# Kernel tuning notes

Measured on AMD Instinct MI355X. Metric: run time of the kernel, lower is better.

Reference implementation:

```python
import jax, jax.numpy as jnp
import numpy as np

D_MODEL = 1024
N_HEADS = 16
D_FF = 4096
EPS = 1e-5


def _linear_init(key, fan_in, fan_out):
    # torch nn.Linear default: U(-1/sqrt(fan_in), 1/sqrt(fan_in))
    k1, k2 = jax.random.split(key)
    bound = 1.0 / np.sqrt(fan_in)
    W = jax.random.uniform(k1, (fan_in, fan_out), minval=-bound, maxval=bound, dtype=jnp.float32)
    b = jax.random.uniform(k2, (fan_out,), minval=-bound, maxval=bound, dtype=jnp.float32)
    return W, b


def setup_inputs() -> dict:
    key = jax.random.key(0)
    ks = jax.random.split(key, 8)
    x = jax.random.normal(ks[0], (4, 2048, D_MODEL), dtype=jnp.float32)
    Wq, bq = _linear_init(ks[1], D_MODEL, D_MODEL)
    Wk, bk = _linear_init(ks[2], D_MODEL, D_MODEL)
    Wv, bv = _linear_init(ks[3], D_MODEL, D_MODEL)
    Wo, bo = _linear_init(ks[4], D_MODEL, D_MODEL)
    W1, b1 = _linear_init(ks[5], D_MODEL, D_FF)
    W2, b2 = _linear_init(ks[6], D_FF, D_MODEL)
    g1 = jnp.ones((D_MODEL,), jnp.float32); be1 = jnp.zeros((D_MODEL,), jnp.float32)
    g2 = jnp.ones((D_MODEL,), jnp.float32); be2 = jnp.zeros((D_MODEL,), jnp.float32)
    return {"x": x, "Wq": Wq, "bq": bq, "Wk": Wk, "bk": bk, "Wv": Wv, "bv": bv,
            "Wo": Wo, "bo": bo, "g1": g1, "be1": be1, "W1": W1, "b1": b1,
            "W2": W2, "b2": b2, "g2": g2, "be2": be2}


def _layernorm(x, g, b):
    mu = jnp.mean(x, axis=-1, keepdims=True)
    var = jnp.mean(jnp.square(x - mu), axis=-1, keepdims=True)
    return (x - mu) * jax.lax.rsqrt(var + EPS) * g + b


def reference(x, Wq, bq, Wk, bk, Wv, bv, Wo, bo, g1, be1, W1, b1, W2, b2, g2, be2):
    B, T, D = x.shape
    H, dk = N_HEADS, D // N_HEADS
    # projections -> [B, H, T, dk]
    def split_heads(y):
        return y.reshape(B, T, H, dk).transpose(0, 2, 1, 3)
    Q = split_heads(x @ Wq + bq)
    K = split_heads(x @ Wk + bk)
    V = split_heads(x @ Wv + bv)
    scores = jnp.einsum('bhtd,bhsd->bhts', Q, K) / jnp.sqrt(jnp.float32(dk))
    weights = jax.nn.softmax(scores, axis=-1)  # no causal mask in original
    ctx = jnp.einsum('bhts,bhsd->bhtd', weights, V)
    ctx = ctx.transpose(0, 2, 1, 3).reshape(B, T, D)
    attn_out = ctx @ Wo + bo
    x = _layernorm(x + attn_out, g1, be1)
    ff = jax.nn.relu(x @ W1 + b1) @ W2 + b2
    x = _layernorm(x + ff, g2, be2)
    return x
```

## Files before the change

### kernel.cpp

```cpp
#include <hip/hip_runtime.h>
#include <hip/hip_bf16.h>
#include <stdint.h>

typedef __attribute__((ext_vector_type(8))) short short8;
typedef __attribute__((ext_vector_type(4))) float f32x4;
typedef __attribute__((ext_vector_type(16))) float f32x16;

#define SEQ 2048
#define DMODEL 1024
#define NH 16
#define DKH 64

__device__ __forceinline__ uint16_t f2b(float f) {
  uint32_t u = __float_as_uint(f);
  uint32_t r = (u + 0x7fff + ((u >> 16) & 1)) >> 16;
  return (uint16_t)r;
}

__device__ __forceinline__ void gload16(const uint16_t* g, uint16_t* l) {
  __builtin_amdgcn_global_load_lds((const __attribute__((address_space(1))) void*)g,
                                   (__attribute__((address_space(3))) void*)l, 16, 0, 0);
}

__global__ __launch_bounds__(256) void k_castx(const float* __restrict__ x,
                                               uint16_t* __restrict__ xb) {
  int i = blockIdx.x * 256 + threadIdx.x;
  float4 v = reinterpret_cast<const float4*>(x)[i];
  uint16_t o[4] = {f2b(v.x), f2b(v.y), f2b(v.z), f2b(v.w)};
  reinterpret_cast<uint2*>(xb)[i] = *reinterpret_cast<uint2*>(o);
}

__global__ __launch_bounds__(256) void k_tcast(const float* __restrict__ W,
                                               uint16_t* __restrict__ Wt, int K, int N) {
  __shared__ float tile[32][33];
  int n0 = blockIdx.x * 32, k0 = blockIdx.y * 32;
  int tx = threadIdx.x & 31, ty = threadIdx.x >> 5;
#pragma unroll
  for (int i = 0; i < 32; i += 8)
    tile[ty + i][tx] = W[(size_t)(k0 + ty + i) * N + n0 + tx];
  __syncthreads();
#pragma unroll
  for (int i = 0; i < 32; i += 8)
    Wt[(size_t)(n0 + ty + i) * K + k0 + tx] = f2b(tile[tx][ty + i]);
}

__global__ __launch_bounds__(256) void k_vtrans(const uint16_t* __restrict__ V,
                                                uint16_t* __restrict__ Vt) {
  __shared__ uint16_t tile[64][72];
  const int s0 = blockIdx.x * 64;
  const uint16_t* Vp = V + (size_t)blockIdx.y * SEQ * DKH;
  uint16_t* Vtp = Vt + (size_t)blockIdx.y * SEQ * DKH;
  const int t = threadIdx.x;
#pragma unroll
  for (int i = t; i < 512; i += 256) {
    int r = i >> 3, c8 = (i & 7) << 3;
    *reinterpret_cast<uint4*>(&tile[r][c8]) =
        *reinterpret_cast<const uint4*>(Vp + (size_t)(s0 + r) * DKH + c8);
  }
  __syncthreads();
#pragma unroll
  for (int i = t; i < 512; i += 256) {
    int d = i >> 3, s8 = (i & 7) << 3;
    uint16_t tmp[8];
#pragma unroll
    for (int j = 0; j < 8; ++j) tmp[j] = tile[s8 + j][d];
    *reinterpret_cast<uint4*>(Vtp + (size_t)d * SEQ + s0 + s8) = *reinterpret_cast<uint4*>(tmp);
  }
}

#define MODE_QKV 0
#define MODE_RAW 1
#define MODE_RELU 2

template <int BN, int MODE>
__global__ __launch_bounds__(512, 2) void k_gemm2(
    const uint16_t* __restrict__ A, const uint16_t* __restrict__ Bt, int M, int N, int K,
    int nx, const float* __restrict__ bias0, const float* __restrict__ bias1,
    const float* __restrict__ bias2, uint16_t* __restrict__ ob0, uint16_t* __restrict__ ob1,
    uint16_t* __restrict__ ob2, float* __restrict__ of) {
  constexpr int ASZ = 256 * 64;
  constexpr int BSZ = BN * 64;
  __shared__ __align__(16) uint16_t lds[2 * (ASZ + BSZ)];
  uint16_t* const Abase = lds;
  uint16_t* const Bbase = lds + 2 * ASZ;
  constexpr int WN = (BN == 256) ? 4 : 2;
  constexpr int MREP = (BN == 256) ? 8 : 4;
  constexpr int NPH = (BN == 256) ? 4 : 2;
  const int o = blockIdx.x;
  const int chunk = gridDim.x >> 3;
  const int wg = (o & 7) * chunk + (o >> 3);
  const int brow = (wg / nx) << 8;
  const int bcol = (wg % nx) * BN;
  const int t = threadIdx.x;
  const int wid = t >> 6, l = t & 63, g = l >> 4, lr = l & 15;
  const int wr = wid / WN, wc = wid % WN;
  const int wrow = wr * (MREP * 16);
  const int wcol = wc * 64;

  const int srow = t >> 3;
  const int ss0 = (t & 7) ^ (srow & 7);
  const int ss1 = (t & 7) ^ ((srow + 64) & 7);

  auto stage_half = [&](const uint16_t* gsrc, int grow0, int kk, uint16_t* ldst) {
    gload16(gsrc + (size_t)(grow0 + srow) * K + kk + ss0 * 8, ldst + t * 8);
    gload16(gsrc + (size_t)(grow0 + srow + 64) * K + kk + ss1 * 8, ldst + 4096 + t * 8);
  };
  auto rdfrag = [&](const uint16_t* buf, int ar, int kk) -> short8 {
    int slot = ((kk << 2) + g) ^ (ar & 7);
    return *reinterpret_cast<const short8*>(buf + ar * 64 + slot * 8);
  };

  f32x4 acc[MREP][4] = {};
  const int nt = K >> 6;

  stage_half(A, brow, 0, Abase);
  stage_half(A, brow + 128, 0, Abase + 8192);
  stage_half(Bt, bcol, 0, Bbase);
  if (BN == 256) stage_half(Bt, bcol + 128, 0, Bbase + 8192);
  __syncthreads();

  for (int kt = 0; kt < nt; ++kt) {
    const int cur = kt & 1;
    const uint16_t* Ac = Abase + cur * ASZ;
    const uint16_t* Bc = Bbase + cur * BSZ;
    uint16_t* An = Abase + (cur ^ 1) * ASZ;
    uint16_t* Bn = Bbase + (cur ^ 1) * BSZ;
    const bool pf = (kt + 1 < nt);
    const int knx = (kt + 1) << 6;
#pragma unroll
    for (int q = 0; q < NPH; ++q) {
      const int mq = (BN == 256) ? (q >> 1) : 0;
      const int nq = (BN == 256) ? (q & 1) : q;
      short8 af[4][2], bf[2][2];
#pragma unroll
      for (int j = 0; j < 4; ++j)
#pragma unroll
        for (int kk = 0; kk < 2; ++kk)
          af[j][kk] = rdfrag(Ac, wrow + (mq * 4 + j) * 16 + lr, kk);
#pragma unroll
      for (int j = 0; j < 2; ++j)
#pragma unroll
        for (int kk = 0; kk < 2; ++kk)
          bf[j][kk] = rdfrag(Bc, wcol + (nq * 2 + j) * 16 + lr, kk);
      if (pf) {
        if (q == 0) {
          stage_half(A, brow, knx, An);
          stage_half(A, brow + 128, knx, An + 8192);
          if (BN == 128) stage_half(Bt, bcol, knx, Bn);
        }
        if (BN == 256 && q == 1) stage_half(Bt, bcol, knx, Bn);
        if (BN == 256 && q == 2) stage_half(Bt, bcol + 128, knx, Bn + 8192);
      }
      __builtin_amdgcn_s_barrier();
      __builtin_amdgcn_s_setprio(1);
#pragma unroll
      for (int j = 0; j < 4; ++j)
#pragma unroll
        for (int j2 = 0; j2 < 2; ++j2)
#pragma unroll
          for (int kk = 0; kk < 2; ++kk)
            acc[mq * 4 + j][nq * 2 + j2] = __builtin_amdgcn_mfma_f32_16x16x32_bf16(
                af[j][kk], bf[j2][kk], acc[mq * 4 + j][nq * 2 + j2], 0, 0, 0);
      __builtin_amdgcn_s_setprio(0);
      if (q == NPH - 1) {
        asm volatile("s_waitcnt vmcnt(0)" ::: "memory");
        __builtin_amdgcn_s_barrier();
        __builtin_amdgcn_sched_barrier(0);
      } else {
        __builtin_amdgcn_s_barrier();
      }
    }
  }

#pragma unroll
  for (int m = 0; m < MREP; ++m) {
#pragma unroll
    for (int n = 0; n < 4; ++n) {
#pragma unroll
      for (int qi = 0; qi < 4; ++qi) {
        int r = brow + wrow + m * 16 + g * 4 + qi;
        int c = bcol + wcol + n * 16 + lr;
        float v = acc[m][n][qi];
        if (MODE == MODE_QKV) {
          int which = c >> 10;
          int hd = c & 1023;
          const float* bp = which == 0 ? bias0 : (which == 1 ? bias1 : bias2);
          v += bp[hd];
          if (which == 0) v *= 0.1803368801f;
          uint16_t* dst = which == 0 ? ob0 : (which == 1 ? ob1 : ob2);
          int b = r >> 11, tt = r & 2047;
          int h = hd >> 6, d = hd & 63;
          dst[((size_t)((b * NH + h) * SEQ + tt)) * DKH + d] = f2b(v);
        } else if (MODE == MODE_RELU) {
          v += bias0[c];
          v = fmaxf(v, 0.0f);
          ob0[(size_t)r * N + c] = f2b(v);
        } else {
          of[(size_t)r * N + c] = v;
        }
      }
    }
  }
}

__global__ __launch_bounds__(256) void k_attn(const uint16_t* __restrict__ Qb,
                                              const uint16_t* __restrict__ Kb,
                                              const uint16_t* __restrict__ Vtg,
                                              uint16_t* __restrict__ ctx) {
  __shared__ __align__(16) uint16_t Ks[2][64 * 64];
  __shared__ __align__(16) uint16_t Vs[2][64 * 64];
  __shared__ float l_arr[4][32];
  const int o = blockIdx.x;
  const int wg = (o & 7) * 128 + (o >> 3);
  const int qt = wg & 15;
  const int bh = wg >> 4;
  const int b = bh >> 4, h = bh & 15;
  const uint16_t* Qp = Qb + (size_t)bh * SEQ * DKH;
  const uint16_t* Kp = Kb + (size_t)bh * SEQ * DKH;
  const uint16_t* Vp = Vtg + (size_t)bh * SEQ * DKH;
  const int t = threadIdx.x, w = t >> 6, l = t & 63;
  const int lo5 = l & 31, hh = l >> 5;
  const int qbase = qt * 128 + w * 32;

  short8 qf[4];
#pragma unroll
  for (int kc = 0; kc < 4; ++kc)
    qf[kc] = *reinterpret_cast<const short8*>(Qp + (size_t)(qbase + lo5) * DKH + kc * 16 + hh * 8);

  f32x16 oacc[2] = {};
  float lsum = 0.f;

  const int swz = ((l & 7) ^ ((l >> 3) & 7)) << 3;
  const int ci0 = w * 2, ci1 = w * 2 + 1;
  const int r0 = ci0 * 8 + (l >> 3), r1 = ci1 * 8 + (l >> 3);
  uint16_t* ldsK0 = &Ks[0][0] + ci0 * 512 + l * 8;
  uint16_t* ldsK1 = &Ks[0][0] + ci1 * 512 + l * 8;
  uint16_t* ldsV0 = &Vs[0][0] + ci0 * 512 + l * 8;
  uint16_t* ldsV1 = &Vs[0][0] + ci1 * 512 + l * 8;
  const uint16_t* gK0 = Kp + (size_t)r0 * DKH + swz;
  const uint16_t* gK1 = Kp + (size_t)r1 * DKH + swz;
  const uint16_t* gV0 = Vp + (size_t)r0 * SEQ + swz;
  const uint16_t* gV1 = Vp + (size_t)r1 * SEQ + swz;

  gload16(gK0, ldsK0);
  gload16(gK1, ldsK1);
  gload16(gV0, ldsV0);
  gload16(gV1, ldsV1);
  __syncthreads();

  for (int tile = 0; tile < 32; ++tile) {
    const int cur = tile & 1;
    if (tile < 31) {
      const int nxt = (cur ^ 1) * 4096;
      const size_t s0n = (size_t)(tile + 1) * 64;
      gload16(gK0 + s0n * DKH, ldsK0 + nxt);
      gload16(gK1 + s0n * DKH, ldsK1 + nxt);
      gload16(gV0 + s0n, ldsV0 + nxt);
      gload16(gV1 + s0n, ldsV1 + nxt);
    }
    const char* Kbuf = reinterpret_cast<const char*>(&Ks[cur][0]);
    const char* Vbuf = reinterpret_cast<const char*>(&Vs[cur][0]);

#pragma unroll
    for (int sblk = 0; sblk < 2; ++sblk) {
      short8 kf[4];
      const int krow = sblk * 32 + lo5;
      const int kxor = (krow & 7) << 4;
#pragma unroll
      for (int kc = 0; kc < 4; ++kc) {
        int cb = (kc * 32 + hh * 16) ^ kxor;
        kf[kc] = *reinterpret_cast<const short8*>(Kbuf + krow * 128 + cb);
      }
      short8 vf[2][2];
#pragma unroll
      for (int scl = 0; scl < 2; ++scl)
#pragma unroll
        for (int dblk = 0; dblk < 2; ++dblk) {
          int vrow = dblk * 32 + lo5;
          int cb = (sblk * 64 + scl * 32 + hh * 16) ^ ((vrow & 7) << 4);
          vf[scl][dblk] = *reinterpret_cast<const short8*>(Vbuf + vrow * 128 + cb);
        }

      f32x16 sa = {};
      __builtin_amdgcn_s_setprio(1);
#pragma unroll
      for (int kc = 0; kc < 4; ++kc)
        sa = __builtin_amdgcn_mfma_f32_32x32x16_bf16(kf[kc], qf[kc], sa, 0, 0, 0);
      __builtin_amdgcn_s_setprio(0);

      float p[16];
      float ls = 0.f;
#pragma unroll
      for (int r = 0; r < 16; ++r) {
        p[r] = __builtin_amdgcn_exp2f(sa[r]);
        ls += p[r];
      }
      lsum += ls;

      uint32_t clo[4], chi[4];
#pragma unroll
      for (int m = 0; m < 4; ++m) {
        asm("v_cvt_pk_bf16_f32 %0, %1, %2" : "=v"(clo[m]) : "v"(p[4 * m]), "v"(p[4 * m + 1]));
        asm("v_cvt_pk_bf16_f32 %0, %1, %2" : "=v"(chi[m]) : "v"(p[4 * m + 2]), "v"(p[4 * m + 3]));
      }

#pragma unroll
      for (int scl = 0; scl < 2; ++scl) {
        uint32_t a0 = clo[2 * scl], b0 = clo[2 * scl + 1];
        uint32_t a1 = chi[2 * scl], b1 = chi[2 * scl + 1];
        asm("v_permlane32_swap_b32 %0, %1" : "+v"(a0), "+v"(b0));
        asm("v_permlane32_swap_b32 %0, %1" : "+v"(a1), "+v"(b1));
        union {
          uint32_t u[4];
          short8 s;
        } pu;
        pu.u[0] = a0;
        pu.u[1] = a1;
        pu.u[2] = b0;
        pu.u[3] = b1;
        __builtin_amdgcn_s_setprio(1);
#pragma unroll
        for (int dblk = 0; dblk < 2; ++dblk)
          oacc[dblk] = __builtin_amdgcn_mfma_f32_32x32x16_bf16(pu.s, vf[scl][dblk], oacc[dblk], 0, 0, 0);
        __builtin_amdgcn_s_setprio(0);
      }
    }
    __syncthreads();
  }

  {
    float full = lsum + __shfl_xor(lsum, 32, 64);
    if (l < 32) l_arr[w][lo5] = full;
  }
#pragma unroll
  for (int r = 0; r < 16; ++r) {
    int q = (r & 3) + 8 * (r >> 2) + 4 * hh;
    float li = 1.0f / l_arr[w][q];
    int rowg = b * SEQ + qbase + q;
#pragma unroll
    for (int dblk = 0; dblk < 2; ++dblk) {
      int colg = h * DKH + dblk * 32 + lo5;
      ctx[(size_t)rowg * DMODEL + colg] = f2b(oacc[dblk][r] * li);
    }
  }
}

template <bool WRITE_B>
__global__ __launch_bounds__(256) void k_ln(const float* __restrict__ in,
                                            const float* __restrict__ bias,
                                            const float* __restrict__ res,
                                            const float* __restrict__ gam,
                                            const float* __restrict__ bet,
                                            float* __restrict__ outf,
                                            uint16_t* __restrict__ outb) {
  const int row = blockIdx.x;
  const int t = threadIdx.x, lane = t & 63, w = t >> 6;
  float4 v = reinterpret_cast<const float4*>(in + (size_t)row * DMODEL)[t];
  float4 bb0 = reinterpret_cast<const float4*>(bias)[t];
  float4 rr = reinterpret_cast<const float4*>(res + (size_t)row * DMODEL)[t];
  v.x += bb0.x + rr.x;
  v.y += bb0.y + rr.y;
  v.z += bb0.z + rr.z;
  v.w += bb0.w + rr.w;
  float s = v.x + v.y + v.z + v.w;
  float s2 = v.x * v.x + v.y * v.y + v.z * v.z + v.w * v.w;
#pragma unroll
  for (int off = 1; off < 64; off <<= 1) {
    s += __shfl_xor(s, off, 64);
    s2 += __shfl_xor(s2, off, 64);
  }
  __shared__ float rs[4], rq[4];
  if (lane == 0) {
    rs[w] = s;
    rq[w] = s2;
  }
  __syncthreads();
  float ts = rs[0] + rs[1] + rs[2] + rs[3];
  float tq = rq[0] + rq[1] + rq[2] + rq[3];
  const float inv = 1.0f / DMODEL;
  float mu = ts * inv;
  float var = tq * inv - mu * mu;
  float rstd = rsqrtf(var + 1e-5f);
  float4 gg = reinterpret_cast<const float4*>(gam)[t];
  float4 bb = reinterpret_cast<const float4*>(bet)[t];
  float4 y;
  y.x = (v.x - mu) * rstd * gg.x + bb.x;
  y.y = (v.y - mu) * rstd * gg.y + bb.y;
  y.z = (v.z - mu) * rstd * gg.z + bb.z;
  y.w = (v.w - mu) * rstd * gg.w + bb.w;
  reinterpret_cast<float4*>(outf)[(size_t)row * 256 + t] = y;
  if (WRITE_B) {
    uint16_t o[4] = {f2b(y.x), f2b(y.y), f2b(y.z), f2b(y.w)};
    reinterpret_cast<uint2*>(outb)[(size_t)row * 256 + t] = *reinterpret_cast<uint2*>(o);
  }
}

extern "C" void kernel_launch(void* const* d_in, const int* in_sizes, int n_in, void* d_out,
                              int out_size, void* d_ws, size_t ws_size, hipStream_t stream) {
  const float* x = (const float*)d_in[0];
  const float* Wq = (const float*)d_in[1];
  const float* bq = (const float*)d_in[2];
  const float* Wk = (const float*)d_in[3];
  const float* bk = (const float*)d_in[4];
  const float* Wv = (const float*)d_in[5];
  const float* bv = (const float*)d_in[6];
  const float* Wo = (const float*)d_in[7];
  const float* bo = (const float*)d_in[8];
  const float* g1 = (const float*)d_in[9];
  const float* be1 = (const float*)d_in[10];
  const float* W1 = (const float*)d_in[11];
  const float* b1 = (const float*)d_in[12];
  const float* W2 = (const float*)d_in[13];
  const float* b2 = (const float*)d_in[14];
  const float* g2 = (const float*)d_in[15];
  const float* be2 = (const float*)d_in[16];

  char* ws = (char*)d_ws;
  size_t off = 0;
  auto alloc = [&](size_t bytes) {
    char* p = ws + off;
    off += (bytes + 255) & ~(size_t)255;
    return p;
  };
  uint16_t* wt_qkv = (uint16_t*)alloc(3072ull * 1024 * 2);
  uint16_t* wt_o = (uint16_t*)alloc(1024ull * 1024 * 2);
  uint16_t* wt_1 = (uint16_t*)alloc(4096ull * 1024 * 2);
  uint16_t* wt_2 = (uint16_t*)alloc(1024ull * 4096 * 2);
  uint16_t* xb = (uint16_t*)alloc(8192ull * 1024 * 2);
  float* sum1 = (float*)alloc(8192ull * 1024 * 4);
  float* x1f = (float*)alloc(8192ull * 1024 * 4);
  char* big = alloc(16777216ull + 67108864ull);
  uint16_t* Qbuf = (uint16_t*)big;
  uint16_t* Kbuf = (uint16_t*)(big + 16777216ull);
  uint16_t* Vbuf = (uint16_t*)(big + 2 * 16777216ull);
  uint16_t* vt = (uint16_t*)x1f;
  uint16_t* ctx = xb;
  uint16_t* x1b = (uint16_t*)big;
  uint16_t* hbuf = (uint16_t*)(big + 16777216ull);
  (void)ws_size;

  k_tcast<<<dim3(32, 32), 256, 0, stream>>>(Wq, wt_qkv, 1024, 1024);
  k_tcast<<<dim3(32, 32), 256, 0, stream>>>(Wk, wt_qkv + 1024 * 1024, 1024, 1024);
  k_tcast<<<dim3(32, 32), 256, 0, stream>>>(Wv, wt_qkv + 2 * 1024 * 1024, 1024, 1024);
  k_tcast<<<dim3(32, 32), 256, 0, stream>>>(Wo, wt_o, 1024, 1024);
  k_tcast<<<dim3(128, 32), 256, 0, stream>>>(W1, wt_1, 1024, 4096);
  k_tcast<<<dim3(32, 128), 256, 0, stream>>>(W2, wt_2, 4096, 1024);
  k_castx<<<8192, 256, 0, stream>>>(x, xb);
  k_gemm2<128, MODE_QKV><<<768, 512, 0, stream>>>(
      xb, wt_qkv, 8192, 3072, 1024, 24, bq, bk, bv, Qbuf, Kbuf, Vbuf, nullptr);
  k_vtrans<<<dim3(32, 64), 256, 0, stream>>>(Vbuf, vt);
  k_attn<<<1024, 256, 0, stream>>>(Qbuf, Kbuf, vt, ctx);
  k_gemm2<128, MODE_RAW><<<256, 512, 0, stream>>>(
      ctx, wt_o, 8192, 1024, 1024, 8, nullptr, nullptr, nullptr, nullptr, nullptr, nullptr, sum1);
  k_ln<true><<<8192, 256, 0, stream>>>(sum1, bo, x, g1, be1, x1f, x1b);
  k_gemm2<256, MODE_RELU><<<512, 512, 0, stream>>>(
      x1b, wt_1, 8192, 4096, 1024, 16, b1, nullptr, nullptr, hbuf, nullptr, nullptr, nullptr);
  k_gemm2<128, MODE_RAW><<<256, 512, 0, stream>>>(
      hbuf, wt_2, 8192, 1024, 4096, 8, nullptr, nullptr, nullptr, nullptr, nullptr, nullptr, sum1);
  k_ln<false><<<8192, 256, 0, stream>>>(sum1, b2, x1f, g2, be2, (float*)d_out, nullptr);
}
```

Baseline: 418.4 us.

## Double query rows per attention wave, fuse weight casts, store bf16 LN residual

Each attention wave now processes two 32-row query blocks against every K/V tile, halving K/V LDS loads per query and halving the grid. The six weight transpose-cast launches are merged into a single kernel to reduce launch overhead. The first LayerNorm no longer writes an fp32 copy, and the second LayerNorm reads the bf16 output as its residual, saving memory traffic but lowering residual precision. The larger attention tile increases register use and lowers the number of blocks per CU.

```diff
diff --git a/kernel.cpp b/kernel.cpp
--- a/kernel.cpp
+++ b/kernel.cpp
@@ -15,6 +15,9 @@
   uint32_t u = __float_as_uint(f);
   uint32_t r = (u + 0x7fff + ((u >> 16) & 1)) >> 16;
   return (uint16_t)r;
+}
+__device__ __forceinline__ float b2f(uint16_t u) {
+  return __uint_as_float(((uint32_t)u) << 16);
 }
 
 __device__ __forceinline__ void gload16(const uint16_t* g, uint16_t* l) {
@@ -30,11 +33,32 @@
   reinterpret_cast<uint2*>(xb)[i] = *reinterpret_cast<uint2*>(o);
 }
 
-__global__ __launch_bounds__(256) void k_tcast(const float* __restrict__ W,
-                                               uint16_t* __restrict__ Wt, int K, int N) {
+__global__ __launch_bounds__(256) void k_tcast_all(
+    const float* __restrict__ Wq, const float* __restrict__ Wk, const float* __restrict__ Wv,
+    const float* __restrict__ Wo, const float* __restrict__ W1, const float* __restrict__ W2,
+    uint16_t* __restrict__ wt_qkv, uint16_t* __restrict__ wt_o, uint16_t* __restrict__ wt_1,
+    uint16_t* __restrict__ wt_2) {
   __shared__ float tile[32][33];
-  int n0 = blockIdx.x * 32, k0 = blockIdx.y * 32;
-  int tx = threadIdx.x & 31, ty = threadIdx.x >> 5;
+  const int id = blockIdx.x;
+  const float* W;
+  uint16_t* Wt;
+  int K, N, bx, by;
+  if (id < 4096) {
+    int wsel = id >> 10, r = id & 1023;
+    K = 1024; N = 1024; bx = r & 31; by = r >> 5;
+    W = wsel == 0 ? Wq : (wsel == 1 ? Wk : (wsel == 2 ? Wv : Wo));
+    Wt = wsel == 3 ? wt_o : wt_qkv + wsel * 1024 * 1024;
+  } else if (id < 8192) {
+    int r = id - 4096;
+    K = 1024; N = 4096; bx = r & 127; by = r >> 7;
+    W = W1; Wt = wt_1;
+  } else {
+    int r = id - 8192;
+    K = 4096; N = 1024; bx = r & 31; by = r >> 5;
+    W = W2; Wt = wt_2;
+  }
+  const int n0 = bx * 32, k0 = by * 32;
+  const int tx = threadIdx.x & 31, ty = threadIdx.x >> 5;
 #pragma unroll
   for (int i = 0; i < 32; i += 8)
     tile[ty + i][tx] = W[(size_t)(k0 + ty + i) * N + n0 + tx];
@@ -209,26 +233,29 @@
                                               uint16_t* __restrict__ ctx) {
   __shared__ __align__(16) uint16_t Ks[2][64 * 64];
   __shared__ __align__(16) uint16_t Vs[2][64 * 64];
-  __shared__ float l_arr[4][32];
+  __shared__ float l_arr[4][2][32];
   const int o = blockIdx.x;
-  const int wg = (o & 7) * 128 + (o >> 3);
-  const int qt = wg & 15;
-  const int bh = wg >> 4;
+  const int wg = (o & 7) * 64 + (o >> 3);
+  const int qt = wg & 7;
+  const int bh = wg >> 3;
   const int b = bh >> 4, h = bh & 15;
   const uint16_t* Qp = Qb + (size_t)bh * SEQ * DKH;
   const uint16_t* Kp = Kb + (size_t)bh * SEQ * DKH;
   const uint16_t* Vp = Vtg + (size_t)bh * SEQ * DKH;
   const int t = threadIdx.x, w = t >> 6, l = t & 63;
   const int lo5 = l & 31, hh = l >> 5;
-  const int qbase = qt * 128 + w * 32;
-
-  short8 qf[4];
-#pragma unroll
-  for (int kc = 0; kc < 4; ++kc)
-    qf[kc] = *reinterpret_cast<const short8*>(Qp + (size_t)(qbase + lo5) * DKH + kc * 16 + hh * 8);
-
-  f32x16 oacc[2] = {};
-  float lsum = 0.f;
+  const int qbase = qt * 256 + w * 64;
+
+  short8 qf[2][4];
+#pragma unroll
+  for (int qb = 0; qb < 2; ++qb)
+#pragma unroll
+    for (int kc = 0; kc < 4; ++kc)
+      qf[qb][kc] = *reinterpret_cast<const short8*>(
+          Qp + (size_t)(qbase + qb * 32 + lo5) * DKH + kc * 16 + hh * 8);
+
+  f32x16 oacc[2][2] = {};
+  float lsum[2] = {0.f, 0.f};
 
   const int swz = ((l & 7) ^ ((l >> 3) & 7)) << 3;
   const int ci0 = w * 2, ci1 = w * 2 + 1;
@@ -281,74 +308,82 @@
           vf[scl][dblk] = *reinterpret_cast<const short8*>(Vbuf + vrow * 128 + cb);
         }
 
-      f32x16 sa = {};
-      __builtin_amdgcn_s_setprio(1);
-#pragma unroll
-      for (int kc = 0; kc < 4; ++kc)
-        sa = __builtin_amdgcn_mfma_f32_32x32x16_bf16(kf[kc], qf[kc], sa, 0, 0, 0);
-      __builtin_amdgcn_s_setprio(0);
-
-      float p[16];
-      float ls = 0.f;
-#pragma unroll
-      for (int r = 0; r < 16; ++r) {
-        p[r] = __builtin_amdgcn_exp2f(sa[r]);
-        ls += p[r];
-      }
-      lsum += ls;
-
-      uint32_t clo[4], chi[4];
-#pragma unroll
-      for (int m = 0; m < 4; ++m) {
-        asm("v_cvt_pk_bf16_f32 %0, %1, %2" : "=v"(clo[m]) : "v"(p[4 * m]), "v"(p[4 * m + 1]));
-        asm("v_cvt_pk_bf16_f32 %0, %1, %2" : "=v"(chi[m]) : "v"(p[4 * m + 2]), "v"(p[4 * m + 3]));
-      }
-
-#pragma unroll
-      for (int scl = 0; scl < 2; ++scl) {
-        uint32_t a0 = clo[2 * scl], b0 = clo[2 * scl + 1];
-        uint32_t a1 = chi[2 * scl], b1 = chi[2 * scl + 1];
-        asm("v_permlane32_swap_b32 %0, %1" : "+v"(a0), "+v"(b0));
-        asm("v_permlane32_swap_b32 %0, %1" : "+v"(a1), "+v"(b1));
-        union {
-          uint32_t u[4];
-          short8 s;
-        } pu;
-        pu.u[0] = a0;
-        pu.u[1] = a1;
-        pu.u[2] = b0;
-        pu.u[3] = b1;
+#pragma unroll
+      for (int qb = 0; qb < 2; ++qb) {
+        f32x16 sa = {};
         __builtin_amdgcn_s_setprio(1);
 #pragma unroll
-        for (int dblk = 0; dblk < 2; ++dblk)
-          oacc[dblk] = __builtin_amdgcn_mfma_f32_32x32x16_bf16(pu.s, vf[scl][dblk], oacc[dblk], 0, 0, 0);
+        for (int kc = 0; kc < 4; ++kc)
+          sa = __builtin_amdgcn_mfma_f32_32x32x16_bf16(kf[kc], qf[qb][kc], sa, 0, 0, 0);
         __builtin_amdgcn_s_setprio(0);
+
+        float p[16];
+        float ls = 0.f;
+#pragma unroll
+        for (int r = 0; r < 16; ++r) {
+          p[r] = __builtin_amdgcn_exp2f(sa[r]);
+          ls += p[r];
+        }
+        lsum[qb] += ls;
+
+        uint32_t clo[4], chi[4];
+#pragma unroll
+        for (int m = 0; m < 4; ++m) {
+          asm("v_cvt_pk_bf16_f32 %0, %1, %2" : "=v"(clo[m]) : "v"(p[4 * m]), "v"(p[4 * m + 1]));
+          asm("v_cvt_pk_bf16_f32 %0, %1, %2" : "=v"(chi[m]) : "v"(p[4 * m + 2]), "v"(p[4 * m + 3]));
+        }
+
+#pragma unroll
+        for (int scl = 0; scl < 2; ++scl) {
+          uint32_t a0 = clo[2 * scl], b0 = clo[2 * scl + 1];
+          uint32_t a1 = chi[2 * scl], b1 = chi[2 * scl + 1];
+          asm("v_permlane32_swap_b32 %0, %1" : "+v"(a0), "+v"(b0));
+          asm("v_permlane32_swap_b32 %0, %1" : "+v"(a1), "+v"(b1));
+          union {
+            uint32_t u[4];
+            short8 s;
+          } pu;
+          pu.u[0] = a0;
+          pu.u[1] = a1;
+          pu.u[2] = b0;
+          pu.u[3] = b1;
+          __builtin_amdgcn_s_setprio(1);
+#pragma unroll
+          for (int dblk = 0; dblk < 2; ++dblk)
+            oacc[qb][dblk] =
+                __builtin_amdgcn_mfma_f32_32x32x16_bf16(pu.s, vf[scl][dblk], oacc[qb][dblk], 0, 0, 0);
+          __builtin_amdgcn_s_setprio(0);
+        }
       }
     }
     __syncthreads();
   }
 
-  {
-    float full = lsum + __shfl_xor(lsum, 32, 64);
-    if (l < 32) l_arr[w][lo5] = full;
-  }
-#pragma unroll
-  for (int r = 0; r < 16; ++r) {
-    int q = (r & 3) + 8 * (r >> 2) + 4 * hh;
-    float li = 1.0f / l_arr[w][q];
-    int rowg = b * SEQ + qbase + q;
-#pragma unroll
-    for (int dblk = 0; dblk < 2; ++dblk) {
-      int colg = h * DKH + dblk * 32 + lo5;
-      ctx[(size_t)rowg * DMODEL + colg] = f2b(oacc[dblk][r] * li);
+#pragma unroll
+  for (int qb = 0; qb < 2; ++qb) {
+    float full = lsum[qb] + __shfl_xor(lsum[qb], 32, 64);
+    if (l < 32) l_arr[w][qb][lo5] = full;
+  }
+#pragma unroll
+  for (int qb = 0; qb < 2; ++qb) {
+#pragma unroll
+    for (int r = 0; r < 16; ++r) {
+      int q = (r & 3) + 8 * (r >> 2) + 4 * hh;
+      float li = 1.0f / l_arr[w][qb][q];
+      int rowg = b * SEQ + qbase + qb * 32 + q;
+#pragma unroll
+      for (int dblk = 0; dblk < 2; ++dblk) {
+        int colg = h * DKH + dblk * 32 + lo5;
+        ctx[(size_t)rowg * DMODEL + colg] = f2b(oacc[qb][dblk][r] * li);
+      }
     }
   }
 }
 
-template <bool WRITE_B>
+template <bool WRITE_B, bool RESBF>
 __global__ __launch_bounds__(256) void k_ln(const float* __restrict__ in,
                                             const float* __restrict__ bias,
-                                            const float* __restrict__ res,
+                                            const void* __restrict__ res,
                                             const float* __restrict__ gam,
                                             const float* __restrict__ bet,
                                             float* __restrict__ outf,
@@ -357,7 +392,17 @@
   const int t = threadIdx.x, lane = t & 63, w = t >> 6;
   float4 v = reinterpret_cast<const float4*>(in + (size_t)row * DMODEL)[t];
   float4 bb0 = reinterpret_cast<const float4*>(bias)[t];
-  float4 rr = reinterpret_cast<const float4*>(res + (size_t)row * DMODEL)[t];
+  float4 rr;
+  if (RESBF) {
+    uint2 ru = reinterpret_cast<const uint2*>((const uint16_t*)res + (size_t)row * DMODEL)[t];
+    const uint16_t* rp = reinterpret_cast<const uint16_t*>(&ru);
+    rr.x = b2f(rp[0]);
+    rr.y = b2f(rp[1]);
+    rr.z = b2f(rp[2]);
+    rr.w = b2f(rp[3]);
+  } else {
+    rr = reinterpret_cast<const float4*>((const float*)res + (size_t)row * DMODEL)[t];
+  }
   v.x += bb0.x + rr.x;
   v.y += bb0.y + rr.y;
   v.z += bb0.z + rr.z;
@@ -388,10 +433,11 @@
   y.y = (v.y - mu) * rstd * gg.y + bb.y;
   y.z = (v.z - mu) * rstd * gg.z + bb.z;
   y.w = (v.w - mu) * rstd * gg.w + bb.w;
-  reinterpret_cast<float4*>(outf)[(size_t)row * 256 + t] = y;
   if (WRITE_B) {
-    uint16_t o[4] = {f2b(y.x), f2b(y.y), f2b(y.z), f2b(y.w)};
-    reinterpret_cast<uint2*>(outb)[(size_t)row * 256 + t] = *reinterpret_cast<uint2*>(o);
+    uint16_t oo[4] = {f2b(y.x), f2b(y.y), f2b(y.z), f2b(y.w)};
+    reinterpret_cast<uint2*>(outb)[(size_t)row * 256 + t] = *reinterpret_cast<uint2*>(oo);
+  } else {
+    reinterpret_cast<float4*>(outf)[(size_t)row * 256 + t] = y;
   }
 }
 
@@ -428,34 +474,28 @@
   uint16_t* wt_2 = (uint16_t*)alloc(1024ull * 4096 * 2);
   uint16_t* xb = (uint16_t*)alloc(8192ull * 1024 * 2);
   float* sum1 = (float*)alloc(8192ull * 1024 * 4);
-  float* x1f = (float*)alloc(8192ull * 1024 * 4);
+  uint16_t* vt = (uint16_t*)alloc(8192ull * 1024 * 2);
   char* big = alloc(16777216ull + 67108864ull);
   uint16_t* Qbuf = (uint16_t*)big;
   uint16_t* Kbuf = (uint16_t*)(big + 16777216ull);
   uint16_t* Vbuf = (uint16_t*)(big + 2 * 16777216ull);
-  uint16_t* vt = (uint16_t*)x1f;
   uint16_t* ctx = xb;
   uint16_t* x1b = (uint16_t*)big;
   uint16_t* hbuf = (uint16_t*)(big + 16777216ull);
   (void)ws_size;
 
-  k_tcast<<<dim3(32, 32), 256, 0, stream>>>(Wq, wt_qkv, 1024, 1024);
-  k_tcast<<<dim3(32, 32), 256, 0, stream>>>(Wk, wt_qkv + 1024 * 1024, 1024, 1024);
-  k_tcast<<<dim3(32, 32), 256, 0, stream>>>(Wv, wt_qkv + 2 * 1024 * 1024, 1024, 1024);
-  k_tcast<<<dim3(32, 32), 256, 0, stream>>>(Wo, wt_o, 1024, 1024);
-  k_tcast<<<dim3(128, 32), 256, 0, stream>>>(W1, wt_1, 1024, 4096);
-  k_tcast<<<dim3(32, 128), 256, 0, stream>>>(W2, wt_2, 4096, 1024);
+  k_tcast_all<<<12288, 256, 0, stream>>>(Wq, Wk, Wv, Wo, W1, W2, wt_qkv, wt_o, wt_1, wt_2);
   k_castx<<<8192, 256, 0, stream>>>(x, xb);
   k_gemm2<128, MODE_QKV><<<768, 512, 0, stream>>>(
       xb, wt_qkv, 8192, 3072, 1024, 24, bq, bk, bv, Qbuf, Kbuf, Vbuf, nullptr);
   k_vtrans<<<dim3(32, 64), 256, 0, stream>>>(Vbuf, vt);
-  k_attn<<<1024, 256, 0, stream>>>(Qbuf, Kbuf, vt, ctx);
+  k_attn<<<512, 256, 0, stream>>>(Qbuf, Kbuf, vt, ctx);
   k_gemm2<128, MODE_RAW><<<256, 512, 0, stream>>>(
       ctx, wt_o, 8192, 1024, 1024, 8, nullptr, nullptr, nullptr, nullptr, nullptr, nullptr, sum1);
-  k_ln<true><<<8192, 256, 0, stream>>>(sum1, bo, x, g1, be1, x1f, x1b);
+  k_ln<true, false><<<8192, 256, 0, stream>>>(sum1, bo, x, g1, be1, nullptr, x1b);
   k_gemm2<256, MODE_RELU><<<512, 512, 0, stream>>>(
       x1b, wt_1, 8192, 4096, 1024, 16, b1, nullptr, nullptr, hbuf, nullptr, nullptr, nullptr);
   k_gemm2<128, MODE_RAW><<<256, 512, 0, stream>>>(
       hbuf, wt_2, 8192, 1024, 4096, 8, nullptr, nullptr, nullptr, nullptr, nullptr, nullptr, sum1);
-  k_ln<false><<<8192, 256, 0, stream>>>(sum1, b2, x1f, g2, be2, (float*)d_out, nullptr);
-}
+  k_ln<false, true><<<8192, 256, 0, stream>>>(sum1, b2, x1b, g2, be2, (float*)d_out, nullptr);
+}
```

New measurement: 421.6 us. Within noise of the previous version (+0.8%).
